# Optimization experiments

Measured on AMD Instinct MI355X. Metric: run time of the kernel, lower is better.

Reference implementation:

```python
import jax, jax.numpy as jnp
import numpy as np

B, T, C = 1, 2048, 2048
H, KV, D = 16, 4, 128
PAST = 2048


def setup_inputs() -> dict:
    key = jax.random.key(0)
    ks = jax.random.split(key, 11)
    return {
        "x": jax.random.normal(ks[0], (B, T, C), jnp.float32),
        "ve": jax.random.normal(ks[1], (B, T, KV * D), jnp.float32),
        "cos": jax.random.normal(ks[2], (1, T, 1, D // 2), jnp.float32),
        "sin": jax.random.normal(ks[3], (1, T, 1, D // 2), jnp.float32),
        "past_key": jax.random.normal(ks[4], (B, PAST, KV, D), jnp.float32),
        "past_value": jax.random.normal(ks[5], (B, PAST, KV, D), jnp.float32),
        "Wq": jax.random.normal(ks[6], (C, H * D), jnp.float32) * 0.02,
        "Wk": jax.random.normal(ks[7], (C, KV * D), jnp.float32) * 0.02,
        "Wv": jax.random.normal(ks[8], (C, KV * D), jnp.float32) * 0.02,
        "Wo": jax.random.normal(ks[9], (H * D, C), jnp.float32) * 0.02,
        "Wg": jax.random.normal(ks[10], (12, KV), jnp.float32),
    }


def _rmsnorm(x):
    return x * jax.lax.rsqrt(jnp.mean(x * x, axis=-1, keepdims=True) + 1e-6)


def _rope(x, cos, sin):
    # x: (B,T,heads,D); cos/sin: (1,T,1,D//2) broadcast over heads
    d = x.shape[-1] // 2
    x1, x2 = x[..., :d], x[..., d:]
    return jnp.concatenate([x1 * cos + x2 * sin, -x1 * sin + x2 * cos], axis=-1)


def reference(x, ve, cos, sin, past_key, past_value, Wq, Wk, Wv, Wo, Wg):
    Bx, Tx, Cx = x.shape
    G = H // KV
    q = (x @ Wq).reshape(Bx, Tx, H, D)
    k = (x @ Wk).reshape(Bx, Tx, KV, D)
    v = (x @ Wv).reshape(Bx, Tx, KV, D)
    # value-embedding gate: 3*sigmoid over first 12 channels of x
    gate = 3.0 * jax.nn.sigmoid(x[..., :12] @ Wg)  # (B,T,KV)
    v = v + gate[..., None] * ve.reshape(Bx, Tx, KV, D)
    q = _rmsnorm(_rope(q, cos, sin)) * 1.2
    k = _rmsnorm(_rope(k, cos, sin)) * 1.2
    present_key = jnp.concatenate([past_key, k], axis=1)    # (B,S,KV,D)
    present_value = jnp.concatenate([past_value, v], axis=1)
    S = present_key.shape[1]
    q_t = q.transpose(0, 2, 1, 3)                           # (B,H,T,D)
    k_t = present_key.transpose(0, 2, 1, 3)                 # (B,KV,S,D)
    v_t = present_value.transpose(0, 2, 1, 3)
    # GQA expansion: repeat each kv head G times -> (B,H,S,D)
    k_t = jnp.broadcast_to(k_t[:, :, None], (Bx, KV, G, S, D)).reshape(Bx, H, S, D)
    v_t = jnp.broadcast_to(v_t[:, :, None], (Bx, KV, G, S, D)).reshape(Bx, H, S, D)
    scale = D ** -0.5
    scores = jnp.einsum("bhtd,bhsd->bhts", q_t, k_t) * scale
    query_pos = jnp.arange(S - Tx, S)[:, None]
    key_pos = jnp.arange(S)[None, :]
    causal = key_pos <= query_pos                           # (T,S)
    scores = jnp.where(causal[None, None], scores, -jnp.inf)
    w = jax.nn.softmax(scores, axis=-1)
    y = jnp.einsum("bhts,bhsd->bthd", w, v_t).reshape(Bx, Tx, H * D)
    y = y @ Wo
    return (y, present_key, present_value)
```

## Files before the change

### kernel.cpp

```cpp
#include <hip/hip_runtime.h>
#include <hip/hip_bf16.h>
#include <math.h>

typedef __attribute__((ext_vector_type(8))) short short8;
typedef __attribute__((ext_vector_type(4))) short short4v;
typedef __attribute__((ext_vector_type(4))) float f32x4;

#define DEV __device__ __forceinline__

DEV short f2bf(float f) {
  unsigned u = __builtin_bit_cast(unsigned, f);
  unsigned r = (u + 0x7FFFu + ((u >> 16) & 1u)) >> 16;
  return (short)r;
}

DEV short f2h(float f) {
  _Float16 h = (_Float16)f;
  return __builtin_bit_cast(short, h);
}

DEV float h2f(short s) {
  return (float)__builtin_bit_cast(_Float16, s);
}

DEV unsigned cvt_pk_bf16(float lo, float hi) {
  unsigned r;
  asm("v_cvt_pk_bf16_f32 %0, %1, %2" : "=v"(r) : "v"(lo), "v"(hi));
  return r;
}

DEV void gload_lds16(const void* g, void* l) {
  __builtin_amdgcn_global_load_lds((const __attribute__((address_space(1))) void*)g,
                                   (__attribute__((address_space(3))) void*)l, 16, 0, 0);
}

__global__ __launch_bounds__(256) void gemm_bf16(const short* __restrict__ A,
                                                 const short* __restrict__ BT,
                                                 float* __restrict__ C,
                                                 int M, int N, int K) {
  __shared__ __attribute__((aligned(16))) short As[2][128 * 32];
  __shared__ __attribute__((aligned(16))) short Bs[2][128 * 32];
  const int tid = threadIdx.x;
  const int w = tid >> 6, l = tid & 63;
  const int g = l >> 4, lr = l & 15;
  const int m0 = blockIdx.y * 128, n0 = blockIdx.x * 128;
  const int wr = w >> 1, wc = w & 1;
  const int q0 = w * 2, q1 = w * 2 + 1;
  const int e0 = q0 * 512 + l * 8, e1 = q1 * 512 + l * 8;
  const int ra = e0 >> 5, ka = e0 & 31;
  const int rb_ = e1 >> 5, kb_ = e1 & 31;
  f32x4 acc[4][4] = {};

  auto stage = [&](int buf, int k0) {
    gload_lds16(A + (size_t)(m0 + ra) * K + k0 + ka, As[buf] + q0 * 512);
    gload_lds16(BT + (size_t)(n0 + ra) * K + k0 + ka, Bs[buf] + q0 * 512);
    gload_lds16(A + (size_t)(m0 + rb_) * K + k0 + kb_, As[buf] + q1 * 512);
    gload_lds16(BT + (size_t)(n0 + rb_) * K + k0 + kb_, Bs[buf] + q1 * 512);
  };

  stage(0, 0);
  __syncthreads();
  int cur = 0;
  for (int k0 = 0; k0 < K; k0 += 32) {
    if (k0 + 32 < K) stage(cur ^ 1, k0 + 32);
    short8 af[4], bfr[4];
#pragma unroll
    for (int i = 0; i < 4; ++i) {
      af[i] = *(const short8*)(As[cur] + (wr * 64 + i * 16 + lr) * 32 + g * 8);
      bfr[i] = *(const short8*)(Bs[cur] + (wc * 64 + i * 16 + lr) * 32 + g * 8);
    }
#pragma unroll
    for (int mi = 0; mi < 4; ++mi)
#pragma unroll
      for (int ni = 0; ni < 4; ++ni)
        acc[mi][ni] = __builtin_amdgcn_mfma_f32_16x16x32_bf16(af[mi], bfr[ni], acc[mi][ni], 0, 0, 0);
    __syncthreads();
    cur ^= 1;
  }
#pragma unroll
  for (int mi = 0; mi < 4; ++mi)
#pragma unroll
    for (int ni = 0; ni < 4; ++ni) {
      int row = m0 + wr * 64 + mi * 16 + g * 4;
      int col = n0 + wc * 64 + ni * 16 + lr;
#pragma unroll
      for (int r = 0; r < 4; ++r)
        C[(size_t)(row + r) * N + col] = acc[mi][ni][r];
    }
}

__global__ __launch_bounds__(256) void transpose_cvt(const float* __restrict__ W,
                                                     short* __restrict__ WT, int N) {
  __shared__ float tile[32][33];
  int tx = threadIdx.x, ty = threadIdx.y;
  int c0 = blockIdx.x * 32, r0 = blockIdx.y * 32;
#pragma unroll
  for (int i = 0; i < 4; ++i)
    tile[ty + i * 8][tx] = W[(size_t)(r0 + ty + i * 8) * N + c0 + tx];
  __syncthreads();
#pragma unroll
  for (int i = 0; i < 4; ++i)
    WT[(size_t)(c0 + ty + i * 8) * 2048 + r0 + tx] = f2bf(tile[tx][ty + i * 8]);
}

__global__ __launch_bounds__(256) void cvt_x(const float* __restrict__ x,
                                             short* __restrict__ xb, int n4) {
  int i = blockIdx.x * 256 + threadIdx.x;
  if (i >= n4) return;
  float4 v = ((const float4*)x)[i];
  short4v o;
  o.x = f2bf(v.x); o.y = f2bf(v.y); o.z = f2bf(v.z); o.w = f2bf(v.w);
  ((short4v*)xb)[i] = o;
}

__global__ __launch_bounds__(256) void qk_post(const float* __restrict__ qkv,
                                               const float* __restrict__ cosb,
                                               const float* __restrict__ sinb,
                                               float* __restrict__ outPK,
                                               short* __restrict__ qb,
                                               short* __restrict__ kb) {
  int gw = (blockIdx.x * 256 + threadIdx.x) >> 6;
  int l = threadIdx.x & 63;
  int t = gw / 20, u = gw - t * 20;
  if (t >= 2048) return;
  float c = cosb[t * 64 + l], s = sinb[t * 64 + l];
  const float* src = qkv + (size_t)t * 3072 + (u < 16 ? u * 128 : 2048 + (u - 16) * 128);
  float x1 = src[l], x2 = src[64 + l];
  float lo = x1 * c + x2 * s;
  float hi = x2 * c - x1 * s;
  float ss = lo * lo + hi * hi;
#pragma unroll
  for (int d = 1; d < 64; d <<= 1) ss += __shfl_xor(ss, d, 64);
  float r = rsqrtf(ss * (1.0f / 128.0f) + 1e-6f) * 1.2f;
  if (u < 16) {
    const float SCQ = 0.08838834764831845f * 1.4426950408889634f;
    float rq = r * SCQ;
    size_t b = ((size_t)u * 2048 + t) * 128;
    qb[b + l] = f2bf(lo * rq);
    qb[b + 64 + l] = f2bf(hi * rq);
  } else {
    lo *= r; hi *= r;
    int kvh = u - 16;
    size_t b = ((size_t)(2048 + t) * 4 + kvh) * 128;
    outPK[b + l] = lo;
    outPK[b + 64 + l] = hi;
    size_t b2 = ((size_t)kvh * 4096 + 2048 + t) * 128;
    kb[b2 + l] = f2bf(lo);
    kb[b2 + 64 + l] = f2bf(hi);
  }
}

__global__ __launch_bounds__(256) void v_gate(const float* __restrict__ qkv,
                                              const float* __restrict__ x,
                                              const float* __restrict__ ve,
                                              const float* __restrict__ Wg,
                                              float* __restrict__ outPV,
                                              short* __restrict__ vbT) {
  int gw = (blockIdx.x * 256 + threadIdx.x) >> 6;
  int l = threadIdx.x & 63;
  int t = gw >> 2, kv = gw & 3;
  float z = 0.f;
#pragma unroll
  for (int j = 0; j < 12; ++j) z += x[(size_t)t * 2048 + j] * Wg[j * 4 + kv];
  float gate = 3.0f / (1.0f + expf(-z));
  const float* vr = qkv + (size_t)t * 3072 + 2560 + kv * 128;
  const float* vei = ve + (size_t)t * 512 + kv * 128;
  float v0 = vr[l] + gate * vei[l];
  float v1 = vr[64 + l] + gate * vei[64 + l];
  size_t b = ((size_t)(2048 + t) * 4 + kv) * 128;
  outPV[b + l] = v0;
  outPV[b + 64 + l] = v1;
  vbT[((size_t)kv * 128 + l) * 4096 + 2048 + t] = f2bf(v0);
  vbT[((size_t)kv * 128 + 64 + l) * 4096 + 2048 + t] = f2bf(v1);
}

__global__ __launch_bounds__(256) void past_copy(const float* __restrict__ pk,
                                                 const float* __restrict__ pv,
                                                 float* __restrict__ outPK,
                                                 float* __restrict__ outPV,
                                                 short* __restrict__ kb,
                                                 short* __restrict__ vbT) {
  int i = blockIdx.x * 256 + threadIdx.x;
  int d = i & 127, kv = (i >> 7) & 3, s = i >> 9;
  float a = pk[i], b = pv[i];
  outPK[i] = a;
  outPV[i] = b;
  kb[((size_t)kv * 4096 + s) * 128 + d] = f2bf(a);
  vbT[((size_t)kv * 128 + d) * 4096 + s] = f2bf(b);
}

__global__ __launch_bounds__(256, 2) void attn(const short* __restrict__ qb,
                                               const short* __restrict__ kb,
                                               const short* __restrict__ vbT,
                                               short* __restrict__ Po,
                                               float* __restrict__ ml) {
  extern __shared__ __attribute__((aligned(16))) short smem[];
  short* Ks = smem;
  short* Vs = smem + 16384;
  const int tid = threadIdx.x, w = tid >> 6, l = tid & 63;
  const int g = l >> 4, lr = l & 15;
  const int lid = blockIdx.x;
  const int qbi = 15 - (lid >> 6);
  const int sub = lid & 63;
  const int h = sub >> 2, cls = sub & 3;
  const int kv = h >> 2;
  const int qw = qbi * 128 + w * 32;
  char* Pw = (char*)(smem + 32768) + w * 2048;
  const short* gK = kb + (size_t)kv * 4096 * 128;
  const short* gV = vbT + (size_t)kv * 128 * 4096;
  const int nT = 34 + 2 * qbi;
  const int cnt = (nT - cls + 3) >> 2;

  short8 aq[2][4];
#pragma unroll
  for (int u = 0; u < 2; ++u)
#pragma unroll
    for (int c4 = 0; c4 < 4; ++c4)
      aq[u][c4] = *(const short8*)(qb + ((size_t)(h * 2048 + qw + u * 16 + lr)) * 128 + c4 * 32 + g * 8);

  float m_r[2] = {-INFINITY, -INFINITY};
  float l_r[2] = {0.f, 0.f};
  f32x4 o[2][8] = {};

  auto stageK = [&](int buf, int s0) {
#pragma unroll
    for (int it = 0; it < 4; ++it) {
      int idx = it * 256 + tid;
      int row = idx >> 4;
      int colB = (idx & 15) * 16;
      int scol = colB ^ ((row & 7) << 4);
      gload_lds16(gK + (size_t)(s0 + row) * 128 + (scol >> 1),
                  Ks + buf * 8192 + (it * 256 + w * 64) * 8);
    }
  };
  auto stageV = [&](int buf, int s0) {
#pragma unroll
    for (int it = 0; it < 4; ++it) {
      int idx = it * 256 + tid;
      int row = idx >> 3;
      int colB = (idx & 7) * 16;
      int scol = colB ^ ((row & 7) << 4);
      gload_lds16(gV + (size_t)row * 4096 + s0 + (scol >> 1),
                  Vs + buf * 8192 + (it * 256 + w * 64) * 8);
    }
  };

  stageK(0, cls * 64);
  stageV(0, cls * 64);
  __syncthreads();
  int cur = 0;
  for (int i = 0; i < cnt; ++i) {
    const int s0 = (cls + 4 * i) * 64;
    if (i + 1 < cnt) {
      stageK(cur ^ 1, s0 + 256);
      stageV(cur ^ 1, s0 + 256);
    }
    f32x4 sc[2][4] = {};
    __builtin_amdgcn_s_setprio(1);
#pragma unroll
    for (int cc = 0; cc < 4; ++cc) {
      const int rb = cur * 8192 + (cc * 16 + lr) * 128;
      short8 bk[4];
#pragma unroll
      for (int c4 = 0; c4 < 4; ++c4)
        bk[c4] = *(const short8*)(Ks + rb + (((c4 * 64 + g * 16) ^ ((lr & 7) << 4)) >> 1));
#pragma unroll
      for (int c4 = 0; c4 < 4; ++c4) {
        sc[0][cc] = __builtin_amdgcn_mfma_f32_16x16x32_bf16(bk[c4], aq[0][c4], sc[0][cc], 0, 0, 0);
        sc[1][cc] = __builtin_amdgcn_mfma_f32_16x16x32_bf16(bk[c4], aq[1][c4], sc[1][cc], 0, 0, 0);
      }
    }
    __builtin_amdgcn_s_setprio(0);
    if (s0 + 63 > 2048 + qw) {
#pragma unroll
      for (int u = 0; u < 2; ++u)
#pragma unroll
        for (int cc = 0; cc < 4; ++cc)
#pragma unroll
          for (int r = 0; r < 4; ++r)
            sc[u][cc][r] = (s0 + cc * 16 + g * 4 + r <= 2048 + qw + u * 16 + lr)
                               ? sc[u][cc][r] : -INFINITY;
    }
    short8 ap[2][2];
#pragma unroll
    for (int u = 0; u < 2; ++u) {
      float pmax = -INFINITY;
#pragma unroll
      for (int cc = 0; cc < 4; ++cc) {
        float a = fmaxf(fmaxf(sc[u][cc][0], sc[u][cc][1]), fmaxf(sc[u][cc][2], sc[u][cc][3]));
        pmax = fmaxf(pmax, a);
      }
      if (!__all(pmax - m_r[u] <= 8.0f)) {
        float tm = fmaxf(pmax, __shfl_xor(pmax, 16, 64));
        tm = fmaxf(tm, __shfl_xor(tm, 32, 64));
        float mn = fmaxf(m_r[u], tm);
        float corr = exp2f(m_r[u] - mn);
        m_r[u] = mn;
        l_r[u] *= corr;
        float co[4];
#pragma unroll
        for (int r = 0; r < 4; ++r) co[r] = __shfl(corr, (l & 48) | (g * 4 + r), 64);
#pragma unroll
        for (int d8 = 0; d8 < 8; ++d8) {
          f32x4 tt = o[u][d8];
#pragma unroll
          for (int r = 0; r < 4; ++r) tt[r] *= co[r];
          o[u][d8] = tt;
        }
      }
      float ps = 0.f;
#pragma unroll
      for (int cc = 0; cc < 4; ++cc) {
        float p0 = exp2f(sc[u][cc][0] - m_r[u]);
        float p1 = exp2f(sc[u][cc][1] - m_r[u]);
        float p2 = exp2f(sc[u][cc][2] - m_r[u]);
        float p3 = exp2f(sc[u][cc][3] - m_r[u]);
        ps += (p0 + p1) + (p2 + p3);
        unsigned pk0 = cvt_pk_bf16(p0, p1);
        unsigned pk1 = cvt_pk_bf16(p2, p3);
        int off8 = (lr * 128 + cc * 32 + g * 8) ^ ((lr & 7) << 4);
        unsigned long long pq = (unsigned long long)pk0 | ((unsigned long long)pk1 << 32);
        *(unsigned long long*)(Pw + off8) = pq;
      }
      l_r[u] += ps;
#pragma unroll
      for (int ks = 0; ks < 2; ++ks)
        ap[u][ks] = *(const short8*)(Pw + ((lr * 128 + ks * 64 + g * 16) ^ ((lr & 7) << 4)));
    }
    __builtin_amdgcn_s_setprio(1);
#pragma unroll
    for (int d8 = 0; d8 < 8; ++d8) {
      const int rb = cur * 8192 + (d8 * 16 + lr) * 64;
      short8 bv0 = *(const short8*)(Vs + rb + (((0 * 64 + g * 16) ^ ((lr & 7) << 4)) >> 1));
      short8 bv1 = *(const short8*)(Vs + rb + (((1 * 64 + g * 16) ^ ((lr & 7) << 4)) >> 1));
      o[0][d8] = __builtin_amdgcn_mfma_f32_16x16x32_bf16(ap[0][0], bv0, o[0][d8], 0, 0, 0);
      o[0][d8] = __builtin_amdgcn_mfma_f32_16x16x32_bf16(ap[0][1], bv1, o[0][d8], 0, 0, 0);
      o[1][d8] = __builtin_amdgcn_mfma_f32_16x16x32_bf16(ap[1][0], bv0, o[1][d8], 0, 0, 0);
      o[1][d8] = __builtin_amdgcn_mfma_f32_16x16x32_bf16(ap[1][1], bv1, o[1][d8], 0, 0, 0);
    }
    __builtin_amdgcn_s_setprio(0);
    __syncthreads();
    cur ^= 1;
  }
#pragma unroll
  for (int u = 0; u < 2; ++u) {
    float ls = l_r[u];
    ls += __shfl_xor(ls, 16, 64);
    ls += __shfl_xor(ls, 32, 64);
    float inv = 1.0f / ls;
    float invo[4];
#pragma unroll
    for (int r = 0; r < 4; ++r) invo[r] = __shfl(inv, (l & 48) | (g * 4 + r), 64);
#pragma unroll
    for (int d8 = 0; d8 < 8; ++d8)
#pragma unroll
      for (int r = 0; r < 4; ++r)
        Po[((size_t)(cls * 16 + h) * 2048 + qw + u * 16 + g * 4 + r) * 128 + d8 * 16 + lr] =
            f2h(o[u][d8][r] * invo[r]);
    if (g == 0) {
      float2 v;
      v.x = m_r[u];
      v.y = ls;
      ((float2*)ml)[(size_t)(cls * 16 + h) * 2048 + qw + u * 16 + lr] = v;
    }
  }
}

__global__ __launch_bounds__(256) void attn_merge(const short* __restrict__ Po,
                                                  const float* __restrict__ ml,
                                                  short* __restrict__ ya) {
  int i = blockIdx.x * 256 + threadIdx.x;
  int q = i >> 8, rem = i & 255, h = rem >> 4, oct = rem & 15;
  float mc[4], lc[4], m = -INFINITY;
#pragma unroll
  for (int c = 0; c < 4; ++c) {
    float2 v = ((const float2*)ml)[(size_t)(c * 16 + h) * 2048 + q];
    mc[c] = v.x; lc[c] = v.y;
    m = fmaxf(m, mc[c]);
  }
  float wsum = 0.f, acc[8] = {};
#pragma unroll
  for (int c = 0; c < 4; ++c) {
    float wc = lc[c] * exp2f(mc[c] - m);
    wsum += wc;
    short8 p = *(const short8*)(Po + ((size_t)(c * 16 + h) * 2048 + q) * 128 + oct * 8);
#pragma unroll
    for (int j = 0; j < 8; ++j) acc[j] += wc * h2f(p[j]);
  }
  float inv = 1.0f / wsum;
  short8 ov;
#pragma unroll
  for (int j = 0; j < 8; ++j) ov[j] = f2bf(acc[j] * inv);
  *(short8*)(ya + (size_t)q * 2048 + h * 128 + oct * 8) = ov;
}

extern "C" void kernel_launch(void* const* d_in, const int* in_sizes, int n_in,
                              void* d_out, int out_size, void* d_ws, size_t ws_size,
                              hipStream_t stream) {
  const float* x = (const float*)d_in[0];
  const float* ve = (const float*)d_in[1];
  const float* cosb = (const float*)d_in[2];
  const float* sinb = (const float*)d_in[3];
  const float* past_key = (const float*)d_in[4];
  const float* past_value = (const float*)d_in[5];
  const float* Wq = (const float*)d_in[6];
  const float* Wk = (const float*)d_in[7];
  const float* Wv = (const float*)d_in[8];
  const float* Wo = (const float*)d_in[9];
  const float* Wg = (const float*)d_in[10];

  float* outY = (float*)d_out;
  float* outPK = outY + 4194304;
  float* outPV = outPK + 2097152;

  short* base = (short*)d_ws;
  short* WToT = base;
  short* WTqkv = base + 4194304;
  short* xb = WTqkv + (size_t)6291456;
  float* qkv = (float*)(xb + (size_t)4194304);
  short* qb = (short*)(qkv + (size_t)6291456);
  short* kb = qb + (size_t)4194304;
  short* vbT = kb + (size_t)2097152;
  short* ya = vbT + (size_t)2097152;
  short* Po = WTqkv;
  float* mlb = (float*)(base + 20971520);

  static bool attr_set = false;
  if (!attr_set) {
    (void)hipFuncSetAttribute((const void*)attn,
                              hipFuncAttributeMaxDynamicSharedMemorySize, 73728);
    attr_set = true;
  }

  cvt_x<<<4096, 256, 0, stream>>>(x, xb, 1048576);
  dim3 tb(32, 8);
  transpose_cvt<<<dim3(64, 64), tb, 0, stream>>>(Wq, WTqkv, 2048);
  transpose_cvt<<<dim3(16, 64), tb, 0, stream>>>(Wk, WTqkv + (size_t)2048 * 2048, 512);
  transpose_cvt<<<dim3(16, 64), tb, 0, stream>>>(Wv, WTqkv + (size_t)2560 * 2048, 512);
  transpose_cvt<<<dim3(64, 64), tb, 0, stream>>>(Wo, WToT, 2048);

  gemm_bf16<<<dim3(24, 16), 256, 0, stream>>>(xb, WTqkv, qkv, 2048, 3072, 2048);

  qk_post<<<10240, 256, 0, stream>>>(qkv, cosb, sinb, outPK, qb, kb);
  v_gate<<<2048, 256, 0, stream>>>(qkv, x, ve, Wg, outPV, vbT);
  past_copy<<<4096, 256, 0, stream>>>(past_key, past_value, outPK, outPV, kb, vbT);

  attn<<<1024, 256, 73728, stream>>>(qb, kb, vbT, Po, mlb);
  attn_merge<<<2048, 256, 0, stream>>>(Po, mlb, ya);

  gemm_bf16<<<dim3(16, 16), 256, 0, stream>>>(ya, WToT, outY, 2048, 2048, 2048);
}
```

Before: 212.9 us.

## Merge prep kernels, coalesce V transpose, add K64 swizzled GEMM with tile remap

The four weight transposes become one launch, and the q/k and v post-processing kernels become one. The scattered strided bf16 writes of V^T are replaced by an LDS-tiled transpose of the present_value output. Both GEMMs get an XCD-aware block remap that groups neighbouring tiles on the same chiplet. The output projection uses a new K=64 kernel with XOR-swizzled LDS to halve barriers and avoid bank conflicts. The cost is one extra read pass over present_value and double the LDS per block in the new GEMM.

```diff
diff --git a/kernel.cpp b/kernel.cpp
--- a/kernel.cpp
+++ b/kernel.cpp
@@ -43,7 +43,11 @@
   const int tid = threadIdx.x;
   const int w = tid >> 6, l = tid & 63;
   const int g = l >> 4, lr = l & 15;
-  const int m0 = blockIdx.y * 128, n0 = blockIdx.x * 128;
+  int nbx = gridDim.x, nwg = nbx * gridDim.y;
+  int flat = blockIdx.y * nbx + blockIdx.x;
+  int qq = nwg >> 3;
+  int f2 = (flat & 7) * qq + (flat >> 3);
+  const int m0 = (f2 / nbx) * 128, n0 = (f2 % nbx) * 128;
   const int wr = w >> 1, wc = w & 1;
   const int q0 = w * 2, q1 = w * 2 + 1;
   const int e0 = q0 * 512 + l * 8, e1 = q1 * 512 + l * 8;
@@ -89,11 +93,88 @@
     }
 }
 
-__global__ __launch_bounds__(256) void transpose_cvt(const float* __restrict__ W,
-                                                     short* __restrict__ WT, int N) {
+__global__ __launch_bounds__(256) void gemm_bf16_k64(const short* __restrict__ A,
+                                                     const short* __restrict__ BT,
+                                                     float* __restrict__ C,
+                                                     int M, int N, int K) {
+  __shared__ __attribute__((aligned(16))) short As[2][128 * 64];
+  __shared__ __attribute__((aligned(16))) short Bs[2][128 * 64];
+  const int tid = threadIdx.x;
+  const int w = tid >> 6, l = tid & 63;
+  const int g = l >> 4, lr = l & 15;
+  int nbx = gridDim.x, nwg = nbx * gridDim.y;
+  int flat = blockIdx.y * nbx + blockIdx.x;
+  int qq = nwg >> 3;
+  int f2 = (flat & 7) * qq + (flat >> 3);
+  const int m0 = (f2 / nbx) * 128, n0 = (f2 % nbx) * 128;
+  const int wr = w >> 1, wc = w & 1;
+  f32x4 acc[4][4] = {};
+
+  auto stage = [&](int buf, int k0) {
+#pragma unroll
+    for (int it = 0; it < 4; ++it) {
+      int idx = it * 256 + tid;
+      int row = idx >> 3;
+      int colB = (idx & 7) * 16;
+      int scol = colB ^ ((row & 7) << 4);
+      gload_lds16(A + (size_t)(m0 + row) * K + k0 + (scol >> 1), As[buf] + idx * 8);
+      gload_lds16(BT + (size_t)(n0 + row) * K + k0 + (scol >> 1), Bs[buf] + idx * 8);
+    }
+  };
+
+  stage(0, 0);
+  __syncthreads();
+  int cur = 0;
+  for (int k0 = 0; k0 < K; k0 += 64) {
+    if (k0 + 64 < K) stage(cur ^ 1, k0 + 64);
+#pragma unroll
+    for (int ki = 0; ki < 2; ++ki) {
+      short8 af[4], bfr[4];
+#pragma unroll
+      for (int i = 0; i < 4; ++i) {
+        int off = ((wr * 64 + i * 16 + lr) * 128 + ((ki * 64 + g * 16) ^ ((lr & 7) << 4))) >> 1;
+        int offb = ((wc * 64 + i * 16 + lr) * 128 + ((ki * 64 + g * 16) ^ ((lr & 7) << 4))) >> 1;
+        af[i] = *(const short8*)(As[cur] + off);
+        bfr[i] = *(const short8*)(Bs[cur] + offb);
+      }
+#pragma unroll
+      for (int mi = 0; mi < 4; ++mi)
+#pragma unroll
+        for (int ni = 0; ni < 4; ++ni)
+          acc[mi][ni] = __builtin_amdgcn_mfma_f32_16x16x32_bf16(af[mi], bfr[ni], acc[mi][ni], 0, 0, 0);
+    }
+    __syncthreads();
+    cur ^= 1;
+  }
+#pragma unroll
+  for (int mi = 0; mi < 4; ++mi)
+#pragma unroll
+    for (int ni = 0; ni < 4; ++ni) {
+      int row = m0 + wr * 64 + mi * 16 + g * 4;
+      int col = n0 + wc * 64 + ni * 16 + lr;
+#pragma unroll
+      for (int r = 0; r < 4; ++r)
+        C[(size_t)(row + r) * N + col] = acc[mi][ni][r];
+    }
+}
+
+__global__ __launch_bounds__(256) void transpose_all(const float* __restrict__ Wq,
+                                                     const float* __restrict__ Wk,
+                                                     const float* __restrict__ Wv,
+                                                     const float* __restrict__ Wo,
+                                                     short* __restrict__ WTqkv,
+                                                     short* __restrict__ WToT) {
   __shared__ float tile[32][33];
+  int bx = blockIdx.x;
+  const float* W;
+  short* WT;
+  int N, cb;
+  if (bx < 64) { W = Wq; WT = WTqkv; N = 2048; cb = bx; }
+  else if (bx < 80) { W = Wk; WT = WTqkv + (size_t)2048 * 2048; N = 512; cb = bx - 64; }
+  else if (bx < 96) { W = Wv; WT = WTqkv + (size_t)2560 * 2048; N = 512; cb = bx - 80; }
+  else { W = Wo; WT = WToT; N = 2048; cb = bx - 96; }
   int tx = threadIdx.x, ty = threadIdx.y;
-  int c0 = blockIdx.x * 32, r0 = blockIdx.y * 32;
+  int c0 = cb * 32, r0 = blockIdx.y * 32;
 #pragma unroll
   for (int i = 0; i < 4; ++i)
     tile[ty + i * 8][tx] = W[(size_t)(r0 + ty + i * 8) * N + c0 + tx];
@@ -113,80 +194,87 @@
   ((short4v*)xb)[i] = o;
 }
 
-__global__ __launch_bounds__(256) void qk_post(const float* __restrict__ qkv,
-                                               const float* __restrict__ cosb,
-                                               const float* __restrict__ sinb,
-                                               float* __restrict__ outPK,
-                                               short* __restrict__ qb,
-                                               short* __restrict__ kb) {
+__global__ __launch_bounds__(256) void qkv_post(const float* __restrict__ qkv,
+                                                const float* __restrict__ cosb,
+                                                const float* __restrict__ sinb,
+                                                const float* __restrict__ x,
+                                                const float* __restrict__ ve,
+                                                const float* __restrict__ Wg,
+                                                float* __restrict__ outPK,
+                                                float* __restrict__ outPV,
+                                                short* __restrict__ qb,
+                                                short* __restrict__ kb) {
   int gw = (blockIdx.x * 256 + threadIdx.x) >> 6;
   int l = threadIdx.x & 63;
-  int t = gw / 20, u = gw - t * 20;
+  int t = gw / 24, u = gw - t * 24;
   if (t >= 2048) return;
-  float c = cosb[t * 64 + l], s = sinb[t * 64 + l];
-  const float* src = qkv + (size_t)t * 3072 + (u < 16 ? u * 128 : 2048 + (u - 16) * 128);
-  float x1 = src[l], x2 = src[64 + l];
-  float lo = x1 * c + x2 * s;
-  float hi = x2 * c - x1 * s;
-  float ss = lo * lo + hi * hi;
-#pragma unroll
-  for (int d = 1; d < 64; d <<= 1) ss += __shfl_xor(ss, d, 64);
-  float r = rsqrtf(ss * (1.0f / 128.0f) + 1e-6f) * 1.2f;
-  if (u < 16) {
-    const float SCQ = 0.08838834764831845f * 1.4426950408889634f;
-    float rq = r * SCQ;
-    size_t b = ((size_t)u * 2048 + t) * 128;
-    qb[b + l] = f2bf(lo * rq);
-    qb[b + 64 + l] = f2bf(hi * rq);
+  if (u < 20) {
+    float c = cosb[t * 64 + l], s = sinb[t * 64 + l];
+    const float* src = qkv + (size_t)t * 3072 + (u < 16 ? u * 128 : 2048 + (u - 16) * 128);
+    float x1 = src[l], x2 = src[64 + l];
+    float lo = x1 * c + x2 * s;
+    float hi = x2 * c - x1 * s;
+    float ss = lo * lo + hi * hi;
+#pragma unroll
+    for (int d = 1; d < 64; d <<= 1) ss += __shfl_xor(ss, d, 64);
+    float r = rsqrtf(ss * (1.0f / 128.0f) + 1e-6f) * 1.2f;
+    if (u < 16) {
+      const float SCQ = 0.08838834764831845f * 1.4426950408889634f;
+      float rq = r * SCQ;
+      size_t b = ((size_t)u * 2048 + t) * 128;
+      qb[b + l] = f2bf(lo * rq);
+      qb[b + 64 + l] = f2bf(hi * rq);
+    } else {
+      lo *= r; hi *= r;
+      int kvh = u - 16;
+      size_t b = ((size_t)(2048 + t) * 4 + kvh) * 128;
+      outPK[b + l] = lo;
+      outPK[b + 64 + l] = hi;
+      size_t b2 = ((size_t)kvh * 4096 + 2048 + t) * 128;
+      kb[b2 + l] = f2bf(lo);
+      kb[b2 + 64 + l] = f2bf(hi);
+    }
   } else {
-    lo *= r; hi *= r;
-    int kvh = u - 16;
-    size_t b = ((size_t)(2048 + t) * 4 + kvh) * 128;
-    outPK[b + l] = lo;
-    outPK[b + 64 + l] = hi;
-    size_t b2 = ((size_t)kvh * 4096 + 2048 + t) * 128;
-    kb[b2 + l] = f2bf(lo);
-    kb[b2 + 64 + l] = f2bf(hi);
-  }
-}
-
-__global__ __launch_bounds__(256) void v_gate(const float* __restrict__ qkv,
-                                              const float* __restrict__ x,
-                                              const float* __restrict__ ve,
-                                              const float* __restrict__ Wg,
-                                              float* __restrict__ outPV,
-                                              short* __restrict__ vbT) {
-  int gw = (blockIdx.x * 256 + threadIdx.x) >> 6;
-  int l = threadIdx.x & 63;
-  int t = gw >> 2, kv = gw & 3;
-  float z = 0.f;
-#pragma unroll
-  for (int j = 0; j < 12; ++j) z += x[(size_t)t * 2048 + j] * Wg[j * 4 + kv];
-  float gate = 3.0f / (1.0f + expf(-z));
-  const float* vr = qkv + (size_t)t * 3072 + 2560 + kv * 128;
-  const float* vei = ve + (size_t)t * 512 + kv * 128;
-  float v0 = vr[l] + gate * vei[l];
-  float v1 = vr[64 + l] + gate * vei[64 + l];
-  size_t b = ((size_t)(2048 + t) * 4 + kv) * 128;
-  outPV[b + l] = v0;
-  outPV[b + 64 + l] = v1;
-  vbT[((size_t)kv * 128 + l) * 4096 + 2048 + t] = f2bf(v0);
-  vbT[((size_t)kv * 128 + 64 + l) * 4096 + 2048 + t] = f2bf(v1);
+    int kv = u - 20;
+    float z = 0.f;
+#pragma unroll
+    for (int j = 0; j < 12; ++j) z += x[(size_t)t * 2048 + j] * Wg[j * 4 + kv];
+    float gate = 3.0f / (1.0f + expf(-z));
+    const float* vr = qkv + (size_t)t * 3072 + 2560 + kv * 128;
+    const float* vei = ve + (size_t)t * 512 + kv * 128;
+    float v0 = vr[l] + gate * vei[l];
+    float v1 = vr[64 + l] + gate * vei[64 + l];
+    size_t b = ((size_t)(2048 + t) * 4 + kv) * 128;
+    outPV[b + l] = v0;
+    outPV[b + 64 + l] = v1;
+  }
 }
 
 __global__ __launch_bounds__(256) void past_copy(const float* __restrict__ pk,
                                                  const float* __restrict__ pv,
                                                  float* __restrict__ outPK,
                                                  float* __restrict__ outPV,
-                                                 short* __restrict__ kb,
-                                                 short* __restrict__ vbT) {
+                                                 short* __restrict__ kb) {
   int i = blockIdx.x * 256 + threadIdx.x;
   int d = i & 127, kv = (i >> 7) & 3, s = i >> 9;
   float a = pk[i], b = pv[i];
   outPK[i] = a;
   outPV[i] = b;
   kb[((size_t)kv * 4096 + s) * 128 + d] = f2bf(a);
-  vbT[((size_t)kv * 128 + d) * 4096 + s] = f2bf(b);
+}
+
+__global__ __launch_bounds__(256) void v_transpose(const float* __restrict__ PV,
+                                                   short* __restrict__ vbT) {
+  __shared__ float tile[32][33];
+  int tx = threadIdx.x, ty = threadIdx.y;
+  int c0 = blockIdx.x * 32, r0 = blockIdx.y * 32;
+#pragma unroll
+  for (int i = 0; i < 4; ++i)
+    tile[ty + i * 8][tx] = PV[(size_t)(r0 + ty + i * 8) * 512 + c0 + tx];
+  __syncthreads();
+#pragma unroll
+  for (int i = 0; i < 4; ++i)
+    vbT[(size_t)(c0 + ty + i * 8) * 4096 + r0 + tx] = f2bf(tile[tx][ty + i * 8]);
 }
 
 __global__ __launch_bounds__(256, 2) void attn(const short* __restrict__ qb,
@@ -433,20 +521,16 @@
   }
 
   cvt_x<<<4096, 256, 0, stream>>>(x, xb, 1048576);
-  dim3 tb(32, 8);
-  transpose_cvt<<<dim3(64, 64), tb, 0, stream>>>(Wq, WTqkv, 2048);
-  transpose_cvt<<<dim3(16, 64), tb, 0, stream>>>(Wk, WTqkv + (size_t)2048 * 2048, 512);
-  transpose_cvt<<<dim3(16, 64), tb, 0, stream>>>(Wv, WTqkv + (size_t)2560 * 2048, 512);
-  transpose_cvt<<<dim3(64, 64), tb, 0, stream>>>(Wo, WToT, 2048);
+  transpose_all<<<dim3(160, 64), dim3(32, 8), 0, stream>>>(Wq, Wk, Wv, Wo, WTqkv, WToT);
 
   gemm_bf16<<<dim3(24, 16), 256, 0, stream>>>(xb, WTqkv, qkv, 2048, 3072, 2048);
 
-  qk_post<<<10240, 256, 0, stream>>>(qkv, cosb, sinb, outPK, qb, kb);
-  v_gate<<<2048, 256, 0, stream>>>(qkv, x, ve, Wg, outPV, vbT);
-  past_copy<<<4096, 256, 0, stream>>>(past_key, past_value, outPK, outPV, kb, vbT);
+  qkv_post<<<12288, 256, 0, stream>>>(qkv, cosb, sinb, x, ve, Wg, outPK, outPV, qb, kb);
+  past_copy<<<4096, 256, 0, stream>>>(past_key, past_value, outPK, outPV, kb);
+  v_transpose<<<dim3(16, 128), dim3(32, 8), 0, stream>>>(outPV, vbT);
 
   attn<<<1024, 256, 73728, stream>>>(qb, kb, vbT, Po, mlb);
   attn_merge<<<2048, 256, 0, stream>>>(Po, mlb, ya);
 
-  gemm_bf16<<<dim3(16, 16), 256, 0, stream>>>(ya, WToT, outY, 2048, 2048, 2048);
-}
+  gemm_bf16_k64<<<dim3(16, 16), 256, 0, stream>>>(ya, WToT, outY, 2048, 2048, 2048);
+}
```

After: 189.5 us. -11.0%, faster.
